# Optimization experiments

Hardware: AMD Instinct MI355X
Metric: run time of the kernel (lower is better)

Reference implementation:

```python
import jax, jax.numpy as jnp
import numpy as np

SMALL = 1e-16
N = 8192      # num_nodes
D_IN = 512    # input_dim
D_LAT = 128   # latent_dim


def setup_inputs() -> dict:
    key = jax.random.key(0)
    ks = jax.random.split(key, 6)
    z = jax.random.normal(ks[0], (N, D_IN), jnp.float32)
    gamma = jax.random.uniform(ks[1], (N, D_IN), jnp.float32)
    delta = jax.random.uniform(ks[2], (N, D_IN), jnp.float32)
    lim = float(np.sqrt(6.0 / (D_IN + D_LAT)))  # glorot-uniform init
    Wz = jax.random.uniform(ks[3], (D_IN, D_LAT), jnp.float32, -lim, lim)
    Wg = jax.random.uniform(ks[4], (D_IN, D_LAT), jnp.float32, -lim, lim)
    Wd = jax.random.uniform(ks[5], (D_IN, D_LAT), jnp.float32, -lim, lim)
    return {
        "z": z, "gamma": gamma, "delta": delta,
        "Wz": Wz, "Wg": Wg, "Wd": Wd,
        "bias": jnp.float32(1.0),
        "w_gam": jnp.float32(0.5),
        "w_del": jnp.float32(0.5),
    }


def reference(z, gamma, delta, Wz, Wg, Wd, bias, w_gam, w_del):
    # column-stochastic transforms (softmax over input_dim axis, as in __init__)
    Tz = jax.nn.softmax(Wz, axis=0)
    Tg = jax.nn.softmax(Wg, axis=0)
    Td = jax.nn.softmax(Wd, axis=0)

    zd = z @ Tz                 # [N, D_LAT]
    gd_raw = gamma @ Tg         # [N, D_LAT]
    dd_raw = delta @ Td         # [N, D_LAT]
    gd = gd_raw + SMALL
    dd = dd_raw + SMALL

    z2 = zd * zd
    # dist_gam[i,j] = sum_k (zd[i,k]-zd[j,k])^2 / gd[i,k]  (sender-scaled)
    # expanded: sum_k z2_i/g_i  +  (1/g_i) . z2_j  -  2 (z_i/g_i) . z_j
    a = jnp.sum(z2 / gd, axis=1)                                  # [N]
    dist_gam = a[:, None] + (1.0 / gd) @ z2.T - 2.0 * (zd / gd) @ zd.T  # [N,N]

    # dist_del[i,j] = sum_k (zd[i,k]-zd[j,k])^2 / dd[j,k]  (receiver-scaled)
    b = jnp.sum(z2 / dd, axis=1)                                  # [N]
    dist_del = z2 @ (1.0 / dd).T - 2.0 * zd @ (zd / dd).T + b[None, :]  # [N,N]

    n = jnp.float32(N)
    x = bias - w_gam * (n * dist_gam) - w_del * (n * dist_del)
    out = jax.nn.sigmoid(x.reshape(-1))                           # [N*N]
    return out, zd, gd_raw, dd_raw
```

## Files before the change

### kernel.cpp

```cpp
#include <hip/hip_runtime.h>
#include <hip/hip_bf16.h>
#include <math.h>


#define NSZ 8192
#define DLAT 128

typedef _Float16 half8 __attribute__((ext_vector_type(8)));
typedef float f32x4 __attribute__((ext_vector_type(4)));

__device__ __forceinline__ void gl_lds16(const void* g, void* l) {
    __builtin_amdgcn_global_load_lds(
        (const __attribute__((address_space(1))) void*)g,
        (__attribute__((address_space(3))) void*)l, 16, 0, 0);
}

__device__ __forceinline__ float fast_sigmoid(float x) {
    float e = __builtin_amdgcn_exp2f(-1.44269504f * x);
    return __builtin_amdgcn_rcpf(1.0f + e);
}

__global__ void softmax_cols(const float* __restrict__ Wz, const float* __restrict__ Wg,
                             const float* __restrict__ Wd, _Float16* __restrict__ Tt) {
    int col = blockIdx.x & 127;
    int m = blockIdx.x >> 7;
    const float* W = (m == 0) ? Wz : (m == 1 ? Wg : Wd);
    _Float16* To = Tt + (size_t)m * 65536 + (size_t)col * 512;
    int l = threadIdx.x;
    float v[8];
    float mx = -3.4e38f;
    for (int i = 0; i < 8; ++i) {
        v[i] = W[(size_t)(i * 64 + l) * 128 + col];
        mx = fmaxf(mx, v[i]);
    }
    for (int off = 32; off; off >>= 1) mx = fmaxf(mx, __shfl_xor(mx, off));
    float s = 0.f;
    for (int i = 0; i < 8; ++i) { v[i] = expf(v[i] - mx); s += v[i]; }
    for (int off = 32; off; off >>= 1) s += __shfl_xor(s, off);
    float inv = 1.0f / s;
    for (int i = 0; i < 8; ++i) To[i * 64 + l] = (_Float16)(v[i] * inv);
}

__global__ __launch_bounds__(128) void gemm3_mfma(const float* __restrict__ z,
                                                  const float* __restrict__ gamma,
                                                  const float* __restrict__ delta,
                                                  const _Float16* __restrict__ Tt,
                                                  float* __restrict__ outTail) {
    int m = blockIdx.y;
    const float* A = (m == 0) ? z : (m == 1 ? gamma : delta);
    const _Float16* B = Tt + (size_t)m * 65536;
    float* C = outTail + (size_t)m * (NSZ * DLAT);
    int rowBase = blockIdx.x * 32;
    __shared__ _Float16 As[32 * 520];
    int t = threadIdx.x;
    for (int s = 0; s < 16; ++s) {
        int id = s * 128 + t;
        int row = id >> 6, c8 = id & 63;
        const float4* src = (const float4*)(A + (size_t)(rowBase + row) * 512 + c8 * 8);
        float4 f0 = src[0], f1 = src[1];
        half8 h = {(_Float16)f0.x, (_Float16)f0.y, (_Float16)f0.z, (_Float16)f0.w,
                   (_Float16)f1.x, (_Float16)f1.y, (_Float16)f1.z, (_Float16)f1.w};
        *(half8*)(&As[row * 520 + c8 * 8]) = h;
    }
    __syncthreads();

    int l = t & 63, w = t >> 6;
    int lc = l & 15, lq = l >> 4;
    int m0 = w * 16;
    f32x4 acc[8] = {};
    for (int kt = 0; kt < 16; ++kt) {
        int k0 = kt * 32;
        half8 af = *(const half8*)(&As[(m0 + lc) * 520 + k0 + lq * 8]);
        for (int ni = 0; ni < 8; ++ni) {
            half8 bf = *(const half8*)(B + (size_t)(ni * 16 + lc) * 512 + k0 + lq * 8);
            acc[ni] = __builtin_amdgcn_mfma_f32_16x16x32_f16(af, bf, acc[ni], 0, 0, 0);
        }
    }
    for (int ni = 0; ni < 8; ++ni) {
        for (int r = 0; r < 4; ++r) {
            int row = rowBase + m0 + lq * 4 + r;
            int col = ni * 16 + lc;
            C[(size_t)row * 128 + col] = acc[ni][r];
        }
    }
}

__global__ void build_stacks(const float* __restrict__ zd, const float* __restrict__ gdr,
                             const float* __restrict__ ddr, _Float16* __restrict__ Afp,
                             _Float16* __restrict__ Bfp, float* __restrict__ cvec,
                             float* __restrict__ bco, const float* __restrict__ pb,
                             const float* __restrict__ pwg, const float* __restrict__ pwd) {
    int i = blockIdx.x;
    int k = threadIdx.x;
    float zv = zd[(size_t)i * 128 + k];
    float g = gdr[(size_t)i * 128 + k] + 1e-16f;
    float d = ddr[(size_t)i * 128 + k] + 1e-16f;
    float z2 = zv * zv;
    float u = 1.0f / g, p = 1.0f / d;
    float v = zv * u, q = zv * p;
    float wg = *pwg, wd = *pwd, bias = *pb;
    _Float16* Ar = Afp + (size_t)i * 512;
    _Float16* Br = Bfp + (size_t)i * 512;
    Ar[k]       = (_Float16)(wg * u);
    Ar[128 + k] = (_Float16)(wg * v);
    Ar[256 + k] = (_Float16)(wd * z2);
    Ar[384 + k] = (_Float16)(wd * zv);
    Br[k]       = (_Float16)(z2);
    Br[128 + k] = (_Float16)(-2.0f * zv);
    Br[256 + k] = (_Float16)(p);
    Br[384 + k] = (_Float16)(-2.0f * q);
    float a = z2 * u, b = z2 * p;
    for (int off = 32; off; off >>= 1) { a += __shfl_down(a, off); b += __shfl_down(b, off); }
    __shared__ float sa[2], sb[2];
    if ((k & 63) == 0) { sa[k >> 6] = a; sb[k >> 6] = b; }
    __syncthreads();
    if (k == 0) {
        cvec[i] = bias - 8192.0f * wg * (sa[0] + sa[1]);
        bco[i] = 8192.0f * wd * (sb[0] + sb[1]);
    }
}

__global__ __launch_bounds__(256) void pair_kernel(const _Float16* __restrict__ Afp,
                                                   const _Float16* __restrict__ Bfp,
                                                   const float* __restrict__ cvec,
                                                   const float* __restrict__ bco,
                                                   const float* __restrict__ pbias,
                                                   float* __restrict__ out) {
    int bid = blockIdx.x;
    int super = bid >> 6, within = bid & 63;
    int sy = super >> 3, sx = super & 7;
    int by = sy * 8 + (within >> 3), bx = sx * 8 + (within & 7);
    int iBase = by * 128, jBase = bx * 128;

    __shared__ _Float16 As[128 * 64];
    __shared__ _Float16 Bs[128 * 64];
    int t = threadIdx.x;
    int l = t & 63, w = t >> 6;
    int wm = (w >> 1) * 64, wn = (w & 1) * 64;
    int lc = l & 15, lq = l >> 4;
    f32x4 acc[4][4] = {};

    int srow = l >> 3;
    int sq = (l & 7) ^ srow;

    for (int kt = 0; kt < 8; ++kt) {
        int k0 = kt * 64;
        for (int s = 0; s < 4; ++s) {
            int rr = (w * 4 + s) * 8 + srow;
            const _Float16* ga = Afp + (size_t)(iBase + rr) * 512 + k0 + sq * 8;
            const _Float16* gb = Bfp + (size_t)(jBase + rr) * 512 + k0 + sq * 8;
            gl_lds16(ga, &As[(w * 4 + s) * 512]);
            gl_lds16(gb, &Bs[(w * 4 + s) * 512]);
        }
        __syncthreads();
        for (int ks = 0; ks < 2; ++ks) {
            half8 af[4], bf[4];
            for (int mi = 0; mi < 4; ++mi) {
                int r = wm + mi * 16 + lc;
                int q = ks * 4 + lq;
                af[mi] = *(const half8*)(&As[((r << 3) + (q ^ (r & 7))) << 3]);
            }
            for (int ni = 0; ni < 4; ++ni) {
                int r = wn + ni * 16 + lc;
                int q = ks * 4 + lq;
                bf[ni] = *(const half8*)(&Bs[((r << 3) + (q ^ (r & 7))) << 3]);
            }
            for (int mi = 0; mi < 4; ++mi)
                for (int ni = 0; ni < 4; ++ni)
                    acc[mi][ni] = __builtin_amdgcn_mfma_f32_16x16x32_f16(af[mi], bf[ni],
                                                                         acc[mi][ni], 0, 0, 0);
        }
        __syncthreads();
    }

    float bias = *pbias;
    float civ[4][4], bjv[4];
    for (int mi = 0; mi < 4; ++mi)
        for (int r = 0; r < 4; ++r)
            civ[mi][r] = cvec[iBase + wm + mi * 16 + lq * 4 + r];
    for (int ni = 0; ni < 4; ++ni) bjv[ni] = bco[jBase + wn + ni * 16 + lc];

    for (int mi = 0; mi < 4; ++mi) {
        for (int ni = 0; ni < 4; ++ni) {
            for (int r = 0; r < 4; ++r) {
                int i = iBase + wm + mi * 16 + lq * 4 + r;
                int j = jBase + wn + ni * 16 + lc;
                float x = civ[mi][r] - bjv[ni] - 8192.0f * acc[mi][ni][r];
                if (i == j) x = bias;
                out[(size_t)i * NSZ + j] = fast_sigmoid(x);
            }
        }
    }
}

extern "C" void kernel_launch(void* const* d_in, const int* in_sizes, int n_in,
                              void* d_out, int out_size, void* d_ws, size_t ws_size,
                              hipStream_t stream) {
    const float* z = (const float*)d_in[0];
    const float* gamma = (const float*)d_in[1];
    const float* delta = (const float*)d_in[2];
    const float* Wz = (const float*)d_in[3];
    const float* Wg = (const float*)d_in[4];
    const float* Wd = (const float*)d_in[5];
    const float* pb = (const float*)d_in[6];
    const float* pwg = (const float*)d_in[7];
    const float* pwd = (const float*)d_in[8];

    float* out = (float*)d_out;
    float* zd_out = out + (size_t)NSZ * NSZ;
    float* gd_out = zd_out + (size_t)NSZ * DLAT;
    float* dd_out = gd_out + (size_t)NSZ * DLAT;

    float* wsf = (float*)d_ws;
    _Float16* Tt = (_Float16*)wsf;
    float* cvec = wsf + 98304;
    float* bco = cvec + 8192;
    _Float16* Afp = (_Float16*)(bco + 8192);
    _Float16* Bfp = Afp + (size_t)NSZ * 512;

    softmax_cols<<<384, 64, 0, stream>>>(Wz, Wg, Wd, Tt);
    gemm3_mfma<<<dim3(256, 3), 128, 0, stream>>>(z, gamma, delta, Tt, zd_out);
    build_stacks<<<NSZ, 128, 0, stream>>>(zd_out, gd_out, dd_out, Afp, Bfp, cvec, bco,
                                          pb, pwg, pwd);
    pair_kernel<<<4096, 256, 0, stream>>>(Afp, Bfp, cvec, bco, pb, out);
}
```

Measured before the change: 428.2 us.

## Fuse projection GEMMs with stack building and use nontemporal output stores

Merges the three projection GEMMs and the build_stacks kernel into one kernel. Each block handles 16 rows across all three inputs and keeps zd and gd in registers, so the build step no longer reads them back from global memory, and one launch is removed. The large sigmoid output and the projection outputs are now written with nontemporal stores to reduce cache pollution. In exchange, the fused kernel runs only 512 blocks with serialized per-matrix phases, which may lower parallelism, and its Afp/Bfp stores are scattered fp16 writes.

```diff
diff --git a/kernel.cpp b/kernel.cpp
--- a/kernel.cpp
+++ b/kernel.cpp
@@ -41,82 +41,100 @@
     for (int i = 0; i < 8; ++i) To[i * 64 + l] = (_Float16)(v[i] * inv);
 }
 
-__global__ __launch_bounds__(128) void gemm3_mfma(const float* __restrict__ z,
-                                                  const float* __restrict__ gamma,
-                                                  const float* __restrict__ delta,
-                                                  const _Float16* __restrict__ Tt,
-                                                  float* __restrict__ outTail) {
-    int m = blockIdx.y;
-    const float* A = (m == 0) ? z : (m == 1 ? gamma : delta);
-    const _Float16* B = Tt + (size_t)m * 65536;
-    float* C = outTail + (size_t)m * (NSZ * DLAT);
-    int rowBase = blockIdx.x * 32;
-    __shared__ _Float16 As[32 * 520];
+__global__ __launch_bounds__(128) void gemm3_build(
+        const float* __restrict__ z, const float* __restrict__ gamma,
+        const float* __restrict__ delta, const _Float16* __restrict__ Tt,
+        float* __restrict__ outTail, _Float16* __restrict__ Afp, _Float16* __restrict__ Bfp,
+        float* __restrict__ cvec, float* __restrict__ bco,
+        const float* __restrict__ pb, const float* __restrict__ pwg,
+        const float* __restrict__ pwd) {
+    int rowBase = blockIdx.x * 16;
+    __shared__ _Float16 As[16 * 520];
+    __shared__ float reds_a[16][2], reds_b[16][2];
     int t = threadIdx.x;
-    for (int s = 0; s < 16; ++s) {
-        int id = s * 128 + t;
-        int row = id >> 6, c8 = id & 63;
-        const float4* src = (const float4*)(A + (size_t)(rowBase + row) * 512 + c8 * 8);
-        float4 f0 = src[0], f1 = src[1];
-        half8 h = {(_Float16)f0.x, (_Float16)f0.y, (_Float16)f0.z, (_Float16)f0.w,
-                   (_Float16)f1.x, (_Float16)f1.y, (_Float16)f1.z, (_Float16)f1.w};
-        *(half8*)(&As[row * 520 + c8 * 8]) = h;
-    }
-    __syncthreads();
-
     int l = t & 63, w = t >> 6;
     int lc = l & 15, lq = l >> 4;
-    int m0 = w * 16;
-    f32x4 acc[8] = {};
-    for (int kt = 0; kt < 16; ++kt) {
-        int k0 = kt * 32;
-        half8 af = *(const half8*)(&As[(m0 + lc) * 520 + k0 + lq * 8]);
-        for (int ni = 0; ni < 8; ++ni) {
-            half8 bf = *(const half8*)(B + (size_t)(ni * 16 + lc) * 512 + k0 + lq * 8);
-            acc[ni] = __builtin_amdgcn_mfma_f32_16x16x32_f16(af, bf, acc[ni], 0, 0, 0);
-        }
-    }
-    for (int ni = 0; ni < 8; ++ni) {
+    float wg = *pwg, wd = *pwd, bias = *pb;
+
+    float vz[4][4], vg[4][4];
+    f32x4 acc[4];
+
+    for (int m = 0; m < 3; ++m) {
+        const float* A = (m == 0) ? z : (m == 1 ? gamma : delta);
+        const _Float16* B = Tt + (size_t)m * 65536;
+        __syncthreads();
+        for (int s = 0; s < 8; ++s) {
+            int id = s * 128 + t;
+            int row = id >> 6, c8 = id & 63;
+            const float4* src = (const float4*)(A + (size_t)(rowBase + row) * 512 + c8 * 8);
+            float4 f0 = src[0], f1 = src[1];
+            half8 h = {(_Float16)f0.x, (_Float16)f0.y, (_Float16)f0.z, (_Float16)f0.w,
+                       (_Float16)f1.x, (_Float16)f1.y, (_Float16)f1.z, (_Float16)f1.w};
+            *(half8*)(&As[row * 520 + c8 * 8]) = h;
+        }
+        __syncthreads();
+        for (int ni = 0; ni < 4; ++ni) acc[ni] = (f32x4){0.f, 0.f, 0.f, 0.f};
+        for (int kt = 0; kt < 16; ++kt) {
+            int k0 = kt * 32;
+            half8 af = *(const half8*)(&As[lc * 520 + k0 + lq * 8]);
+            for (int ni = 0; ni < 4; ++ni) {
+                int j = w * 64 + ni * 16 + lc;
+                half8 bf = *(const half8*)(B + (size_t)j * 512 + k0 + lq * 8);
+                acc[ni] = __builtin_amdgcn_mfma_f32_16x16x32_f16(af, bf, acc[ni], 0, 0, 0);
+            }
+        }
+        float* C = outTail + (size_t)m * (NSZ * DLAT);
+        for (int ni = 0; ni < 4; ++ni) {
+            for (int r = 0; r < 4; ++r) {
+                int row = rowBase + lq * 4 + r;
+                int col = w * 64 + ni * 16 + lc;
+                __builtin_nontemporal_store(acc[ni][r], &C[(size_t)row * 128 + col]);
+                if (m == 0) vz[ni][r] = acc[ni][r];
+                else if (m == 1) vg[ni][r] = acc[ni][r];
+            }
+        }
+    }
+
+    float pa[4] = {0.f, 0.f, 0.f, 0.f}, pbv[4] = {0.f, 0.f, 0.f, 0.f};
+    for (int ni = 0; ni < 4; ++ni) {
         for (int r = 0; r < 4; ++r) {
-            int row = rowBase + m0 + lq * 4 + r;
-            int col = ni * 16 + lc;
-            C[(size_t)row * 128 + col] = acc[ni][r];
-        }
-    }
-}
-
-__global__ void build_stacks(const float* __restrict__ zd, const float* __restrict__ gdr,
-                             const float* __restrict__ ddr, _Float16* __restrict__ Afp,
-                             _Float16* __restrict__ Bfp, float* __restrict__ cvec,
-                             float* __restrict__ bco, const float* __restrict__ pb,
-                             const float* __restrict__ pwg, const float* __restrict__ pwd) {
-    int i = blockIdx.x;
-    int k = threadIdx.x;
-    float zv = zd[(size_t)i * 128 + k];
-    float g = gdr[(size_t)i * 128 + k] + 1e-16f;
-    float d = ddr[(size_t)i * 128 + k] + 1e-16f;
-    float z2 = zv * zv;
-    float u = 1.0f / g, p = 1.0f / d;
-    float v = zv * u, q = zv * p;
-    float wg = *pwg, wd = *pwd, bias = *pb;
-    _Float16* Ar = Afp + (size_t)i * 512;
-    _Float16* Br = Bfp + (size_t)i * 512;
-    Ar[k]       = (_Float16)(wg * u);
-    Ar[128 + k] = (_Float16)(wg * v);
-    Ar[256 + k] = (_Float16)(wd * z2);
-    Ar[384 + k] = (_Float16)(wd * zv);
-    Br[k]       = (_Float16)(z2);
-    Br[128 + k] = (_Float16)(-2.0f * zv);
-    Br[256 + k] = (_Float16)(p);
-    Br[384 + k] = (_Float16)(-2.0f * q);
-    float a = z2 * u, b = z2 * p;
-    for (int off = 32; off; off >>= 1) { a += __shfl_down(a, off); b += __shfl_down(b, off); }
-    __shared__ float sa[2], sb[2];
-    if ((k & 63) == 0) { sa[k >> 6] = a; sb[k >> 6] = b; }
+            int i = rowBase + lq * 4 + r;
+            int k = w * 64 + ni * 16 + lc;
+            float zv = vz[ni][r];
+            float g = vg[ni][r] + 1e-16f;
+            float d = acc[ni][r] + 1e-16f;
+            float z2 = zv * zv;
+            float u = 1.0f / g, p = 1.0f / d;
+            _Float16* Ar = Afp + (size_t)i * 512;
+            _Float16* Br = Bfp + (size_t)i * 512;
+            Ar[k]       = (_Float16)(wg * u);
+            Ar[128 + k] = (_Float16)(wg * zv * u);
+            Ar[256 + k] = (_Float16)(wd * z2);
+            Ar[384 + k] = (_Float16)(wd * zv);
+            Br[k]       = (_Float16)(z2);
+            Br[128 + k] = (_Float16)(-2.0f * zv);
+            Br[256 + k] = (_Float16)(p);
+            Br[384 + k] = (_Float16)(-2.0f * zv * p);
+            pa[r] += z2 * u;
+            pbv[r] += z2 * p;
+        }
+    }
+    for (int r = 0; r < 4; ++r) {
+        for (int off = 8; off; off >>= 1) {
+            pa[r] += __shfl_xor(pa[r], off);
+            pbv[r] += __shfl_xor(pbv[r], off);
+        }
+    }
+    if (lc == 0) {
+        for (int r = 0; r < 4; ++r) {
+            reds_a[lq * 4 + r][w] = pa[r];
+            reds_b[lq * 4 + r][w] = pbv[r];
+        }
+    }
     __syncthreads();
-    if (k == 0) {
-        cvec[i] = bias - 8192.0f * wg * (sa[0] + sa[1]);
-        bco[i] = 8192.0f * wd * (sb[0] + sb[1]);
+    if (t < 16) {
+        cvec[rowBase + t] = bias - 8192.0f * wg * (reds_a[t][0] + reds_a[t][1]);
+        bco[rowBase + t] = 8192.0f * wd * (reds_b[t][0] + reds_b[t][1]);
     }
 }
 
@@ -187,7 +205,7 @@
                 int j = jBase + wn + ni * 16 + lc;
                 float x = civ[mi][r] - bjv[ni] - 8192.0f * acc[mi][ni][r];
                 if (i == j) x = bias;
-                out[(size_t)i * NSZ + j] = fast_sigmoid(x);
+                __builtin_nontemporal_store(fast_sigmoid(x), &out[(size_t)i * NSZ + j]);
             }
         }
     }
@@ -208,8 +226,6 @@
 
     float* out = (float*)d_out;
     float* zd_out = out + (size_t)NSZ * NSZ;
-    float* gd_out = zd_out + (size_t)NSZ * DLAT;
-    float* dd_out = gd_out + (size_t)NSZ * DLAT;
 
     float* wsf = (float*)d_ws;
     _Float16* Tt = (_Float16*)wsf;
@@ -219,8 +235,7 @@
     _Float16* Bfp = Afp + (size_t)NSZ * 512;
 
     softmax_cols<<<384, 64, 0, stream>>>(Wz, Wg, Wd, Tt);
-    gemm3_mfma<<<dim3(256, 3), 128, 0, stream>>>(z, gamma, delta, Tt, zd_out);
-    build_stacks<<<NSZ, 128, 0, stream>>>(zd_out, gd_out, dd_out, Afp, Bfp, cvec, bco,
-                                          pb, pwg, pwd);
+    gemm3_build<<<512, 128, 0, stream>>>(z, gamma, delta, Tt, zd_out, Afp, Bfp,
+                                         cvec, bco, pb, pwg, pwd);
     pair_kernel<<<4096, 256, 0, stream>>>(Afp, Bfp, cvec, bco, pb, out);
 }
```

New measurement: 443.7 us. 3.6% more time.
